# Optimization experiments

Hardware: AMD Instinct MI355X
Metric: run time of the kernel (lower is better)

The kernel has to match this reference:

```python
import jax, jax.numpy as jnp
import numpy as np

CHANNELS = 1024
T_LEN = 16384
WINDOW = 16
W_MIN, W_MAX = -1.0, 3.0
BETA = 0.95       # snn.Leaky(beta=0.95)
THRESHOLD = 1.0   # snn.Leaky(threshold=1)


def setup_inputs() -> dict:
    key = jax.random.key(0)
    inp = jax.random.normal(key, (CHANNELS, T_LEN), dtype=jnp.float32)
    return {"inp": inp}


def reference(inp):
    C, T = inp.shape
    pad = WINDOW // 2
    inp_padded = jnp.pad(inp, ((0, 0), (pad, pad)))  # [C, T + WINDOW]
    n_steps = T - WINDOW

    def step(carry, t):
        w, mem = carry
        # B: sliding window [C, WINDOW] starting at column t of padded input
        B = jax.lax.dynamic_slice(inp_padded, (0, t), (C, WINDOW))
        # mean(B @ B.T, axis=1) == B @ mean(B, axis=0)  -- avoids [C, C] intermediate
        B_ram = B @ jnp.mean(B, axis=0)
        w = jnp.clip(0.5 * w + 0.5 * B_ram, W_MIN, W_MAX)
        x = B[:, 0]  # == inp_padded[:, t]
        # snntorch Leaky, reset_mechanism='subtract':
        # reset from incoming mem, then mem = beta*mem + input - reset*thr, spk = mem > thr
        reset = (mem > THRESHOLD).astype(inp.dtype)
        mem = BETA * mem + w * x - reset * THRESHOLD
        spk = (mem > THRESHOLD).astype(inp.dtype)
        return (w, mem), spk

    w0 = jnp.ones((C,), dtype=inp.dtype)
    mem0 = jnp.zeros((C,), dtype=inp.dtype)
    _, spks = jax.lax.scan(step, (w0, mem0), jnp.arange(n_steps))  # spks: [n_steps, C]
    # out = deepcopy(inp); out[:, t] = spk for t < T - WINDOW
    out = inp.at[:, :n_steps].set(spks.T)
    return out
```

## Files before the change

### kernel.cpp

```cpp
#include <hip/hip_runtime.h>

#define C_CH   1024
#define T_DIM  16384
#define NSTEPS (T_DIM - 16)
#define PAD    8
#define TP     (T_DIM + 16)
#define CHUNK  512
#define NCHUNK 32
#define WARM   256
#define LPITCH 17

#define WS_CM_OFFSET (8u * T_DIM * sizeof(double))

__global__ void colsum_partial(const float* __restrict__ inp, double* __restrict__ part) {
    int col = blockIdx.x * 256 + threadIdx.x;
    int rc  = blockIdx.y;
    const float* p = inp + (size_t)rc * 128 * T_DIM + col;
    double a0=0,a1=0,a2=0,a3=0,a4=0,a5=0,a6=0,a7=0;
    #pragma unroll
    for (int r = 0; r < 128; r += 8) {
        a0 += (double)p[(size_t)(r+0) * T_DIM];
        a1 += (double)p[(size_t)(r+1) * T_DIM];
        a2 += (double)p[(size_t)(r+2) * T_DIM];
        a3 += (double)p[(size_t)(r+3) * T_DIM];
        a4 += (double)p[(size_t)(r+4) * T_DIM];
        a5 += (double)p[(size_t)(r+5) * T_DIM];
        a6 += (double)p[(size_t)(r+6) * T_DIM];
        a7 += (double)p[(size_t)(r+7) * T_DIM];
    }
    part[(size_t)rc * T_DIM + col] = ((a0+a1)+(a2+a3)) + ((a4+a5)+(a6+a7));
}

__global__ void colmean_tail(const double* __restrict__ part, const float* __restrict__ inp,
                             float* __restrict__ cm, float* __restrict__ out) {
    int i = blockIdx.x * 256 + threadIdx.x;
    if (i < TP) {
        float v = 0.0f;
        if (i >= PAD && i < T_DIM + PAD) {
            int col = i - PAD;
            double t = 0.0;
            #pragma unroll
            for (int r = 0; r < 8; ++r) t += part[(size_t)r * T_DIM + col];
            v = (float)(t * (1.0 / 1024.0));
        }
        cm[i] = v;
    }
    if (i < C_CH * 16) {
        int c = i >> 4, j = i & 15;
        size_t idx = (size_t)c * T_DIM + NSTEPS + j;
        out[idx] = inp[idx];
    }
}

__global__ __launch_bounds__(128) void scan_kernel(const float* __restrict__ inp,
                                                   const float* __restrict__ cm,
                                                   float* __restrict__ out) {
    __shared__ float xt[128][LPITCH];
    __shared__ float st[128][LPITCH];

    const int k    = blockIdx.x;
    const int lane = threadIdx.x;
    const int c0   = blockIdx.y * 128;
    const int t0   = k * CHUNK;
    const int tend = min(t0 + CHUNK, NSTEPS);
    const int tw   = (t0 - WARM > 0) ? (t0 - WARM) : 0;

    const int sr  = lane >> 2;
    const int sc4 = (lane & 3) << 2;
    const float* srow0 = inp + (size_t)(c0 + sr)      * T_DIM + sc4 + 8;
    const float* srow1 = inp + (size_t)(c0 + sr + 32) * T_DIM + sc4 + 8;
    const float* srow2 = inp + (size_t)(c0 + sr + 64) * T_DIM + sc4 + 8;
    const float* srow3 = inp + (size_t)(c0 + sr + 96) * T_DIM + sc4 + 8;
    float* orow0 = out + (size_t)(c0 + sr)      * T_DIM + sc4;
    float* orow1 = out + (size_t)(c0 + sr + 32) * T_DIM + sc4;
    float* orow2 = out + (size_t)(c0 + sr + 64) * T_DIM + sc4;
    float* orow3 = out + (size_t)(c0 + sr + 96) * T_DIM + sc4;

    float4 r0, r1, r2, r3;
    if (tw == 0 && sc4 < 8) {
        r0 = r1 = r2 = r3 = make_float4(0.f, 0.f, 0.f, 0.f);
    } else {
        r0 = *(const float4*)(srow0 + tw - 16);
        r1 = *(const float4*)(srow1 + tw - 16);
        r2 = *(const float4*)(srow2 + tw - 16);
        r3 = *(const float4*)(srow3 + tw - 16);
    }
    xt[sr][sc4+0]    = r0.x; xt[sr][sc4+1]    = r0.y; xt[sr][sc4+2]    = r0.z; xt[sr][sc4+3]    = r0.w;
    xt[sr+32][sc4+0] = r1.x; xt[sr+32][sc4+1] = r1.y; xt[sr+32][sc4+2] = r1.z; xt[sr+32][sc4+3] = r1.w;
    xt[sr+64][sc4+0] = r2.x; xt[sr+64][sc4+1] = r2.y; xt[sr+64][sc4+2] = r2.z; xt[sr+64][sc4+3] = r2.w;
    xt[sr+96][sc4+0] = r3.x; xt[sr+96][sc4+1] = r3.y; xt[sr+96][sc4+2] = r3.z; xt[sr+96][sc4+3] = r3.w;
    __syncthreads();

    float xs[16];
    float win = 0.0f;
    #pragma unroll
    for (int j = 0; j < 16; ++j) {
        float x = xt[lane][j];
        xs[j] = x;
        win = fmaf(x, cm[tw + j], win);
    }
    float w = 1.0f, mem = 0.0f;
    __syncthreads();

    r0 = *(const float4*)(srow0 + tw);
    r1 = *(const float4*)(srow1 + tw);
    r2 = *(const float4*)(srow2 + tw);
    r3 = *(const float4*)(srow3 + tw);

    for (int t = tw; t < tend; t += 16) {
        xt[sr][sc4+0]    = r0.x; xt[sr][sc4+1]    = r0.y; xt[sr][sc4+2]    = r0.z; xt[sr][sc4+3]    = r0.w;
        xt[sr+32][sc4+0] = r1.x; xt[sr+32][sc4+1] = r1.y; xt[sr+32][sc4+2] = r1.z; xt[sr+32][sc4+3] = r1.w;
        xt[sr+64][sc4+0] = r2.x; xt[sr+64][sc4+1] = r2.y; xt[sr+64][sc4+2] = r2.z; xt[sr+64][sc4+3] = r2.w;
        xt[sr+96][sc4+0] = r3.x; xt[sr+96][sc4+1] = r3.y; xt[sr+96][sc4+2] = r3.z; xt[sr+96][sc4+3] = r3.w;
        __syncthreads();

        int ts = (t + 16 < tend) ? (t + 16) : t;
        r0 = *(const float4*)(srow0 + ts);
        r1 = *(const float4*)(srow1 + ts);
        r2 = *(const float4*)(srow2 + ts);
        r3 = *(const float4*)(srow3 + ts);

        #pragma unroll
        for (int j = 0; j < 16; ++j) {
            w = fminf(fmaxf(fmaf(0.5f, w, 0.5f * win), -1.0f), 3.0f);
            float x   = xs[j];
            float rst = (mem > 1.0f) ? 1.0f : 0.0f;
            mem = fmaf(0.95f, mem, fmaf(w, x, -rst));
            st[lane][j] = (mem > 1.0f) ? 1.0f : 0.0f;
            float xn = xt[lane][j];
            win = fmaf(xn, cm[t + 16 + j], fmaf(-x, cm[t + j], win));
            xs[j] = xn;
        }
        __syncthreads();

        if (t >= t0) {
            *(float4*)(orow0 + t) = make_float4(st[sr][sc4],    st[sr][sc4+1],    st[sr][sc4+2],    st[sr][sc4+3]);
            *(float4*)(orow1 + t) = make_float4(st[sr+32][sc4], st[sr+32][sc4+1], st[sr+32][sc4+2], st[sr+32][sc4+3]);
            *(float4*)(orow2 + t) = make_float4(st[sr+64][sc4], st[sr+64][sc4+1], st[sr+64][sc4+2], st[sr+64][sc4+3]);
            *(float4*)(orow3 + t) = make_float4(st[sr+96][sc4], st[sr+96][sc4+1], st[sr+96][sc4+2], st[sr+96][sc4+3]);
        }
        __syncthreads();
    }
}

extern "C" void kernel_launch(void* const* d_in, const int* in_sizes, int n_in,
                              void* d_out, int out_size, void* d_ws, size_t ws_size,
                              hipStream_t stream) {
    const float* inp = (const float*)d_in[0];
    float* out = (float*)d_out;
    double* part = (double*)d_ws;
    float* cm = (float*)((char*)d_ws + WS_CM_OFFSET);

    colsum_partial<<<dim3(T_DIM / 256, 8), 256, 0, stream>>>(inp, part);
    colmean_tail<<<dim3(65), 256, 0, stream>>>(part, inp, cm, out);
    scan_kernel<<<dim3(NCHUNK, C_CH / 128), 128, 0, stream>>>(inp, cm, out);
}
```

Baseline: 161.3 us.

## Use 64-thread blocks, smaller chunks and 32-step tiles in the scan kernel

The scan kernel now runs one 64-lane wavefront per block, covering 64 channels, with the time chunk halved to 256 and twice as many chunks. That raises the block count from 256 to 1024 so more CUs are busy during the sequential recurrence. Each staging step now loads 32 time columns per row instead of 16, which halves the number of barriers per time step, and adds bounds guards for the partial final tile. The cost is that the 256-step warm-up now equals the chunk length, so each block does about twice as much redundant recurrence work relative to the output it keeps.

```diff
diff --git a/kernel.cpp b/kernel.cpp
--- a/kernel.cpp
+++ b/kernel.cpp
@@ -5,10 +5,11 @@
 #define NSTEPS (T_DIM - 16)
 #define PAD    8
 #define TP     (T_DIM + 16)
-#define CHUNK  512
-#define NCHUNK 32
+#define CHUNK  256
+#define NCHUNK 64
 #define WARM   256
-#define LPITCH 17
+#define STEP   32
+#define LP     33
 
 #define WS_CM_OFFSET (8u * T_DIM * sizeof(double))
 
@@ -52,92 +53,100 @@
     }
 }
 
-__global__ __launch_bounds__(128) void scan_kernel(const float* __restrict__ inp,
-                                                   const float* __restrict__ cm,
-                                                   float* __restrict__ out) {
-    __shared__ float xt[128][LPITCH];
-    __shared__ float st[128][LPITCH];
+__global__ __launch_bounds__(64) void scan_kernel(const float* __restrict__ inp,
+                                                  const float* __restrict__ cm,
+                                                  float* __restrict__ out) {
+    __shared__ float xt[64][LP];
+    __shared__ float st[64][LP];
 
     const int k    = blockIdx.x;
     const int lane = threadIdx.x;
-    const int c0   = blockIdx.y * 128;
+    const int c0   = blockIdx.y * 64;
     const int t0   = k * CHUNK;
     const int tend = min(t0 + CHUNK, NSTEPS);
     const int tw   = (t0 - WARM > 0) ? (t0 - WARM) : 0;
 
-    const int sr  = lane >> 2;
-    const int sc4 = (lane & 3) << 2;
-    const float* srow0 = inp + (size_t)(c0 + sr)      * T_DIM + sc4 + 8;
-    const float* srow1 = inp + (size_t)(c0 + sr + 32) * T_DIM + sc4 + 8;
-    const float* srow2 = inp + (size_t)(c0 + sr + 64) * T_DIM + sc4 + 8;
-    const float* srow3 = inp + (size_t)(c0 + sr + 96) * T_DIM + sc4 + 8;
-    float* orow0 = out + (size_t)(c0 + sr)      * T_DIM + sc4;
-    float* orow1 = out + (size_t)(c0 + sr + 32) * T_DIM + sc4;
-    float* orow2 = out + (size_t)(c0 + sr + 64) * T_DIM + sc4;
-    float* orow3 = out + (size_t)(c0 + sr + 96) * T_DIM + sc4;
+    const int r16 = lane >> 2;
+    const int c4  = (lane & 3) << 2;
+    const int r8  = lane >> 3;
+    const int c8  = (lane & 7) << 2;
 
-    float4 r0, r1, r2, r3;
-    if (tw == 0 && sc4 < 8) {
-        r0 = r1 = r2 = r3 = make_float4(0.f, 0.f, 0.f, 0.f);
-    } else {
-        r0 = *(const float4*)(srow0 + tw - 16);
-        r1 = *(const float4*)(srow1 + tw - 16);
-        r2 = *(const float4*)(srow2 + tw - 16);
-        r3 = *(const float4*)(srow3 + tw - 16);
+    {
+        bool zf = (tw == 0) && (c4 < 8);
+        #pragma unroll
+        for (int h = 0; h < 4; ++h) {
+            int r = r16 + 16 * h;
+            float4 v = make_float4(0.f, 0.f, 0.f, 0.f);
+            if (!zf) v = *(const float4*)(inp + (size_t)(c0 + r) * T_DIM + (tw - 8 + c4));
+            xt[r][c4+0] = v.x; xt[r][c4+1] = v.y; xt[r][c4+2] = v.z; xt[r][c4+3] = v.w;
+        }
     }
-    xt[sr][sc4+0]    = r0.x; xt[sr][sc4+1]    = r0.y; xt[sr][sc4+2]    = r0.z; xt[sr][sc4+3]    = r0.w;
-    xt[sr+32][sc4+0] = r1.x; xt[sr+32][sc4+1] = r1.y; xt[sr+32][sc4+2] = r1.z; xt[sr+32][sc4+3] = r1.w;
-    xt[sr+64][sc4+0] = r2.x; xt[sr+64][sc4+1] = r2.y; xt[sr+64][sc4+2] = r2.z; xt[sr+64][sc4+3] = r2.w;
-    xt[sr+96][sc4+0] = r3.x; xt[sr+96][sc4+1] = r3.y; xt[sr+96][sc4+2] = r3.z; xt[sr+96][sc4+3] = r3.w;
     __syncthreads();
 
-    float xs[16];
+    float dl[16];
     float win = 0.0f;
     #pragma unroll
     for (int j = 0; j < 16; ++j) {
         float x = xt[lane][j];
-        xs[j] = x;
+        dl[j] = x;
         win = fmaf(x, cm[tw + j], win);
     }
     float w = 1.0f, mem = 0.0f;
     __syncthreads();
 
-    r0 = *(const float4*)(srow0 + tw);
-    r1 = *(const float4*)(srow1 + tw);
-    r2 = *(const float4*)(srow2 + tw);
-    r3 = *(const float4*)(srow3 + tw);
+    const float* gp[8];
+    float*       op[8];
+    #pragma unroll
+    for (int g = 0; g < 8; ++g) {
+        gp[g] = inp + (size_t)(c0 + r8 + 8 * g) * T_DIM + 8 + c8;
+        op[g] = out + (size_t)(c0 + r8 + 8 * g) * T_DIM + c8;
+    }
 
-    for (int t = tw; t < tend; t += 16) {
-        xt[sr][sc4+0]    = r0.x; xt[sr][sc4+1]    = r0.y; xt[sr][sc4+2]    = r0.z; xt[sr][sc4+3]    = r0.w;
-        xt[sr+32][sc4+0] = r1.x; xt[sr+32][sc4+1] = r1.y; xt[sr+32][sc4+2] = r1.z; xt[sr+32][sc4+3] = r1.w;
-        xt[sr+64][sc4+0] = r2.x; xt[sr+64][sc4+1] = r2.y; xt[sr+64][sc4+2] = r2.z; xt[sr+64][sc4+3] = r2.w;
-        xt[sr+96][sc4+0] = r3.x; xt[sr+96][sc4+1] = r3.y; xt[sr+96][sc4+2] = r3.z; xt[sr+96][sc4+3] = r3.w;
+    float4 pf[8];
+    {
+        int toff = (tw + c8 <= T_DIM - 12) ? tw : 0;
+        #pragma unroll
+        for (int g = 0; g < 8; ++g) pf[g] = *(const float4*)(gp[g] + toff);
+    }
+
+    for (int t = tw; t < tend; t += STEP) {
+        #pragma unroll
+        for (int g = 0; g < 8; ++g) {
+            int r = r8 + 8 * g;
+            xt[r][c8+0] = pf[g].x; xt[r][c8+1] = pf[g].y; xt[r][c8+2] = pf[g].z; xt[r][c8+3] = pf[g].w;
+        }
         __syncthreads();
 
-        int ts = (t + 16 < tend) ? (t + 16) : t;
-        r0 = *(const float4*)(srow0 + ts);
-        r1 = *(const float4*)(srow1 + ts);
-        r2 = *(const float4*)(srow2 + ts);
-        r3 = *(const float4*)(srow3 + ts);
+        {
+            int tn = t + STEP;
+            int toff = (tn < tend && tn + c8 <= T_DIM - 12) ? tn : 0;
+            #pragma unroll
+            for (int g = 0; g < 8; ++g) pf[g] = *(const float4*)(gp[g] + toff);
+        }
 
+        int jn = tend - t;
         #pragma unroll
-        for (int j = 0; j < 16; ++j) {
-            w = fminf(fmaxf(fmaf(0.5f, w, 0.5f * win), -1.0f), 3.0f);
-            float x   = xs[j];
-            float rst = (mem > 1.0f) ? 1.0f : 0.0f;
-            mem = fmaf(0.95f, mem, fmaf(w, x, -rst));
-            st[lane][j] = (mem > 1.0f) ? 1.0f : 0.0f;
-            float xn = xt[lane][j];
-            win = fmaf(xn, cm[t + 16 + j], fmaf(-x, cm[t + j], win));
-            xs[j] = xn;
+        for (int j = 0; j < STEP; ++j) {
+            if (j < jn) {
+                w = fminf(fmaxf(fmaf(0.5f, w, 0.5f * win), -1.0f), 3.0f);
+                float x   = dl[j & 15];
+                float rst = (mem > 1.0f) ? 1.0f : 0.0f;
+                mem = fmaf(0.95f, mem, fmaf(w, x, -rst));
+                st[lane][j] = (mem > 1.0f) ? 1.0f : 0.0f;
+                float xn = xt[lane][j];
+                win = fmaf(xn, cm[t + 16 + j], fmaf(-x, cm[t + j], win));
+                dl[j & 15] = xn;
+            }
         }
         __syncthreads();
 
         if (t >= t0) {
-            *(float4*)(orow0 + t) = make_float4(st[sr][sc4],    st[sr][sc4+1],    st[sr][sc4+2],    st[sr][sc4+3]);
-            *(float4*)(orow1 + t) = make_float4(st[sr+32][sc4], st[sr+32][sc4+1], st[sr+32][sc4+2], st[sr+32][sc4+3]);
-            *(float4*)(orow2 + t) = make_float4(st[sr+64][sc4], st[sr+64][sc4+1], st[sr+64][sc4+2], st[sr+64][sc4+3]);
-            *(float4*)(orow3 + t) = make_float4(st[sr+96][sc4], st[sr+96][sc4+1], st[sr+96][sc4+2], st[sr+96][sc4+3]);
+            #pragma unroll
+            for (int g = 0; g < 8; ++g) {
+                int r = r8 + 8 * g;
+                if (t + c8 < tend)
+                    *(float4*)(op[g] + t) = make_float4(st[r][c8], st[r][c8+1], st[r][c8+2], st[r][c8+3]);
+            }
         }
         __syncthreads();
     }
@@ -153,5 +162,5 @@
 
     colsum_partial<<<dim3(T_DIM / 256, 8), 256, 0, stream>>>(inp, part);
     colmean_tail<<<dim3(65), 256, 0, stream>>>(part, inp, cm, out);
-    scan_kernel<<<dim3(NCHUNK, C_CH / 128), 128, 0, stream>>>(inp, cm, out);
+    scan_kernel<<<dim3(NCHUNK, C_CH / 64), 64, 0, stream>>>(inp, cm, out);
 }
```

Result: no change. 159.1 us (-1.3%).
